# Kernel tuning notes

Measured on AMD Instinct MI355X. Metric: run time of the kernel, lower is better.

## Reference

```python
import jax, jax.numpy as jnp
import numpy as np
from jax import lax

B, C_IN, L = 16, 4, 300000
KERNEL, ANCHOR_N = 11, 16
LEAK = 1e-4
EPS = 1e-12  # torch F.normalize eps


def setup_inputs() -> dict:
    key = jax.random.key(0)
    k1, k2, k3 = jax.random.split(key, 3)
    data = jax.random.normal(k1, (B, C_IN, L), dtype=jnp.float32)
    # Conv1d weights, PyTorch default init scale ~ U(-s, s), s = 1/sqrt(fan_in)
    s = 1.0 / np.sqrt(C_IN * KERNEL)
    W = jax.random.uniform(k2, (ANCHOR_N, C_IN, KERNEL), dtype=jnp.float32, minval=-s, maxval=s)
    b = jax.random.uniform(k3, (ANCHOR_N,), dtype=jnp.float32, minval=-s, maxval=s)
    return {"data": data, "W": W, "b": b, "anchor_index": 3}


def reference(data, W, b, anchor_index):
    # Conv1d(4 -> anchor_n, valid padding) + LeakyReLU(0.0001)
    y = lax.conv_general_dilated(
        data, W, window_strides=(1,), padding="VALID",
        dimension_numbers=("NCH", "OIH", "NCH"))
    y = y + b[None, :, None]                      # [B, anchor_n, Lc]
    y = jnp.where(y > 0, y, LEAK * y)
    # select anchor channel, add leading dim -> [1, B, Lc]
    ch = y[:, anchor_index, :][None]
    # F.normalize(dim=2, p=1)
    denom = jnp.maximum(jnp.sum(jnp.abs(ch), axis=2, keepdims=True), EPS)
    channel = ch / denom
    # softmax over sequence dim (gamma = 1)
    dist = jax.nn.softmax(channel, axis=2)
    # weighted moments of position distribution (single pass each)
    Lc = dist.shape[2]
    x = jnp.arange(Lc, dtype=dist.dtype)          # positions
    mean = jnp.sum(dist * x, axis=2, keepdims=True)    # [1,B,1]
    x_diff = x - mean                                   # [1,B,Lc]
    var = jnp.sum(dist * x_diff * x_diff, axis=2, keepdims=True)
    z = x_diff / jnp.sqrt(var)
    z3 = z * z * z
    skews = jnp.mean(z3, axis=2)                  # [1,B]
    kts = jnp.mean(z3 * z, axis=2) - 3.0          # [1,B]
    return (skews, kts, channel)
```

## Files before the change

### kernel.cpp

```cpp
#include <hip/hip_runtime.h>
#include <hip/hip_cooperative_groups.h>
#include <math.h>

namespace cg = cooperative_groups;

#define BATCH 16
#define CIN 4
#define LEN 300000
#define KW 11
#define LC (LEN - KW + 1)
#define LCP 300000
#define LEAK 1e-4f
#define EPS_N 1e-12f

#define TPB 256
#define EPT 4
#define NBX 64
#define NBLK (NBX * BATCH)
#define CHUNK 4688
#define ITER 5


__device__ inline void conv_iter_fast(const float* __restrict__ src,
                                      const float* w, float sb, float* yo)
{
    float acc0 = sb, acc1 = sb, acc2 = sb, acc3 = sb;
#pragma unroll
    for (int c = 0; c < CIN; ++c) {
        const float* s = src + (size_t)c * LEN;
        const float4 v0 = *(const float4*)(s);
        const float4 v1 = *(const float4*)(s + 4);
        const float4 v2 = *(const float4*)(s + 8);
        const float4 v3 = *(const float4*)(s + 12);
        float x[16] = { v0.x, v0.y, v0.z, v0.w,  v1.x, v1.y, v1.z, v1.w,
                        v2.x, v2.y, v2.z, v2.w,  v3.x, v3.y, v3.z, v3.w };
#pragma unroll
        for (int k = 0; k < KW; ++k) {
            const float wv = w[c * KW + k];
            acc0 = fmaf(x[k],     wv, acc0);
            acc1 = fmaf(x[k + 1], wv, acc1);
            acc2 = fmaf(x[k + 2], wv, acc2);
            acc3 = fmaf(x[k + 3], wv, acc3);
        }
    }
    yo[0] = acc0 > 0.0f ? acc0 : LEAK * acc0;
    yo[1] = acc1 > 0.0f ? acc1 : LEAK * acc1;
    yo[2] = acc2 > 0.0f ? acc2 : LEAK * acc2;
    yo[3] = acc3 > 0.0f ? acc3 : LEAK * acc3;
}

__device__ inline float conv_one(const float* __restrict__ dbase, int l,
                                 const float* w, float sb)
{
    float acc = sb;
#pragma unroll
    for (int c = 0; c < CIN; ++c)
#pragma unroll
        for (int k = 0; k < KW; ++k)
            acc = fmaf(dbase[(size_t)c * LEN + l + k], w[c * KW + k], acc);
    return acc > 0.0f ? acc : LEAK * acc;
}

__device__ inline void finalize_row(double e, double m1, double m2,
                                    float* __restrict__ out, int b)
{
    const double mean = m1 / e;
    const double var  = m2 / e - mean * mean;

    const double n   = (double)LC;
    const double nm1 = n - 1.0;
    const double S1p = 0.5 * n * nm1;
    const double S2p = nm1 * n * (2.0 * n - 1.0) / 6.0;
    const double S3p = S1p * S1p;
    const double S4p = S2p * (3.0 * n * n - 3.0 * n - 1.0) / 5.0;

    const double mu  = mean;
    const double mu2 = mu * mu;
    const double P3 = S3p - 3.0 * mu * S2p + 3.0 * mu2 * S1p - n * mu * mu2;
    const double P4 = S4p - 4.0 * mu * S3p + 6.0 * mu2 * S2p
                      - 4.0 * mu * mu2 * S1p + n * mu2 * mu2;

    const double sv = sqrt(var);
    out[b]         = (float)(P3 / (n * sv * sv * sv));
    out[BATCH + b] = (float)(P4 / (n * var * var) - 3.0);
}

__global__ __launch_bounds__(256, 4) void fused(
    const float* __restrict__ data, const float* __restrict__ W,
    const float* __restrict__ bias, const int* __restrict__ aidx,
    float* __restrict__ out,
    double* __restrict__ absP, float* __restrict__ maxP, double* __restrict__ sP)
{
    cg::grid_group grid = cg::this_grid();

    const int b = blockIdx.y, j = blockIdx.x, tid = threadIdx.x;
    const int a = aidx[0];

    float w[CIN * KW];
#pragma unroll
    for (int k = 0; k < CIN * KW; ++k) w[k] = W[a * CIN * KW + k];
    const float sb = bias[a];

    const float* dbase = data + (size_t)b * (CIN * (size_t)LEN);
    const int cstart = j * CHUNK;
    const int cend   = min(cstart + CHUNK, LC);

    float y[ITER][EPT];
    float aabs = 0.0f, amax = -INFINITY;

#pragma unroll
    for (int it = 0; it < ITER; ++it) {
        const int o = cstart + it * (TPB * EPT) + tid * EPT;
        if (o + EPT <= cend && o + 16 <= LEN) {
            conv_iter_fast(dbase + o, w, sb, y[it]);
            aabs += (fabsf(y[it][0]) + fabsf(y[it][1])) +
                    (fabsf(y[it][2]) + fabsf(y[it][3]));
            amax = fmaxf(amax, fmaxf(fmaxf(y[it][0], y[it][1]),
                                     fmaxf(y[it][2], y[it][3])));
        } else {
#pragma unroll
            for (int u = 0; u < EPT; ++u) {
                const int l = o + u;
                if (l < cend) {
                    const float v = conv_one(dbase, l, w, sb);
                    y[it][u] = v;
                    aabs += fabsf(v);
                    amax = fmaxf(amax, v);
                }
            }
        }
    }

#pragma unroll
    for (int off = 32; off; off >>= 1) {
        aabs += __shfl_down(aabs, off);
        amax = fmaxf(amax, __shfl_down(amax, off));
    }
    __shared__ float ra[4], rm[4];
    const int wv = tid >> 6;
    if ((tid & 63) == 0) { ra[wv] = aabs; rm[wv] = amax; }
    __syncthreads();
    if (tid == 0) {
        absP[b * NBX + j] = (double)((ra[0] + ra[1]) + (ra[2] + ra[3]));
        maxP[b * NBX + j] = fmaxf(fmaxf(rm[0], rm[1]), fmaxf(rm[2], rm[3]));
    }

    grid.sync();

    __shared__ float sstat[2];
    if (tid < 64) {
        double s = absP[b * NBX + tid];
        float  m = maxP[b * NBX + tid];
#pragma unroll
        for (int off = 32; off; off >>= 1) {
            s += __shfl_down(s, off);
            m = fmaxf(m, __shfl_down(m, off));
        }
        if (tid == 0) {
            sstat[0] = fmaxf((float)s, EPS_N);
            sstat[1] = m;
        }
    }
    __syncthreads();
    const float inv = 1.0f / sstat[0];
    const float mx  = sstat[1] * inv;

    float* dst = out + 2 * BATCH + (size_t)b * LC;

    double te = 0.0, t1 = 0.0, t2 = 0.0;

#pragma unroll
    for (int it = 0; it < ITER; ++it) {
        const int o = cstart + it * (TPB * EPT) + tid * EPT;
        if (o + EPT <= cend && o + 16 <= LEN) {
            const float c0 = y[it][0] * inv, c1 = y[it][1] * inv;
            const float c2 = y[it][2] * inv, c3 = y[it][3] * inv;
            if ((b & 1) == 0) {
                *(float4*)(dst + o) = make_float4(c0, c1, c2, c3);
            } else {
                *(float2*)(dst + o)     = make_float2(c0, c1);
                *(float2*)(dst + o + 2) = make_float2(c2, c3);
            }
            const float e0 = expf(c0 - mx), e1 = expf(c1 - mx);
            const float e2 = expf(c2 - mx), e3 = expf(c3 - mx);
            const float se  = (e0 + e1) + (e2 + e3);
            const float su  = e1 + 2.0f * e2 + 3.0f * e3;
            const float suu = e1 + 4.0f * e2 + 9.0f * e3;
            const double od = (double)o;
            te += (double)se;
            t1 += od * (double)se + (double)su;
            t2 += od * od * (double)se + 2.0 * od * (double)su + (double)suu;
        } else {
#pragma unroll
            for (int u = 0; u < EPT; ++u) {
                const int l = o + u;
                if (l < cend) {
                    const float c = y[it][u] * inv;
                    dst[l] = c;
                    const float e = expf(c - mx);
                    const double xd = (double)l;
                    te += (double)e;
                    t1 += (double)e * xd;
                    t2 += (double)e * xd * xd;
                }
            }
        }
    }

#pragma unroll
    for (int off = 32; off; off >>= 1) {
        te += __shfl_down(te, off);
        t1 += __shfl_down(t1, off);
        t2 += __shfl_down(t2, off);
    }
    __shared__ double we[4], w1[4], w2[4];
    if ((tid & 63) == 0) { we[wv] = te; w1[wv] = t1; w2[wv] = t2; }
    __syncthreads();
    if (tid == 0) {
        double* p = sP + (size_t)(b * NBX + j) * 3;
        p[0] = (we[0] + we[1]) + (we[2] + we[3]);
        p[1] = (w1[0] + w1[1]) + (w1[2] + w1[3]);
        p[2] = (w2[0] + w2[1]) + (w2[2] + w2[3]);
    }

    grid.sync();

    if (j == 0 && tid < 64) {
        const double* p = sP + (size_t)(b * NBX + tid) * 3;
        double e = p[0], m1 = p[1], m2 = p[2];
#pragma unroll
        for (int off = 32; off; off >>= 1) {
            e  += __shfl_down(e, off);
            m1 += __shfl_down(m1, off);
            m2 += __shfl_down(m2, off);
        }
        if (tid == 0) finalize_row(e, m1, m2, out, b);
    }
}

__global__ __launch_bounds__(256) void conv_stats_fb(
    const float* __restrict__ data, const float* __restrict__ W,
    const float* __restrict__ bias, const int* __restrict__ aidx,
    float* __restrict__ ch, double* __restrict__ absP, float* __restrict__ maxP)
{
    const int b = blockIdx.y, j = blockIdx.x, tid = threadIdx.x;
    const int a = aidx[0];
    float w[CIN * KW];
#pragma unroll
    for (int k = 0; k < CIN * KW; ++k) w[k] = W[a * CIN * KW + k];
    const float sb = bias[a];

    const float* dbase = data + (size_t)b * (CIN * (size_t)LEN);
    float* chrow = ch + (size_t)b * LCP;
    const int cstart = j * CHUNK;
    const int cend   = min(cstart + CHUNK, LC);

    float aabs = 0.0f, amax = -INFINITY;
#pragma unroll
    for (int it = 0; it < ITER; ++it) {
        const int o = cstart + it * (TPB * EPT) + tid * EPT;
        if (o + EPT <= cend && o + 16 <= LEN) {
            float yv[EPT];
            conv_iter_fast(dbase + o, w, sb, yv);
            *(float4*)(chrow + o) = make_float4(yv[0], yv[1], yv[2], yv[3]);
            aabs += (fabsf(yv[0]) + fabsf(yv[1])) + (fabsf(yv[2]) + fabsf(yv[3]));
            amax = fmaxf(amax, fmaxf(fmaxf(yv[0], yv[1]), fmaxf(yv[2], yv[3])));
        } else {
            for (int l = o; l < min(o + EPT, cend); ++l) {
                const float v = conv_one(dbase, l, w, sb);
                chrow[l] = v;
                aabs += fabsf(v);
                amax = fmaxf(amax, v);
            }
        }
    }

#pragma unroll
    for (int off = 32; off; off >>= 1) {
        aabs += __shfl_down(aabs, off);
        amax = fmaxf(amax, __shfl_down(amax, off));
    }
    __shared__ float ra[4], rm[4];
    const int wv = tid >> 6;
    if ((tid & 63) == 0) { ra[wv] = aabs; rm[wv] = amax; }
    __syncthreads();
    if (tid == 0) {
        absP[b * NBX + j] = (double)((ra[0] + ra[1]) + (ra[2] + ra[3]));
        maxP[b * NBX + j] = fmaxf(fmaxf(rm[0], rm[1]), fmaxf(rm[2], rm[3]));
    }
}

__global__ __launch_bounds__(256) void softmax_fb(
    const float* __restrict__ ch, const double* __restrict__ absP,
    const float* __restrict__ maxP, float* __restrict__ chan_out,
    double* __restrict__ sP)
{
    const int b = blockIdx.y, j = blockIdx.x, tid = threadIdx.x;

    __shared__ float sstat[2];
    if (tid < 64) {
        double s = absP[b * NBX + tid];
        float  m = maxP[b * NBX + tid];
#pragma unroll
        for (int off = 32; off; off >>= 1) {
            s += __shfl_down(s, off);
            m = fmaxf(m, __shfl_down(m, off));
        }
        if (tid == 0) { sstat[0] = fmaxf((float)s, EPS_N); sstat[1] = m; }
    }
    __syncthreads();
    const float inv = 1.0f / sstat[0];
    const float mx  = sstat[1] * inv;

    const float* src = ch + (size_t)b * LCP;
    float* dst = chan_out + (size_t)b * LC;
    const int cstart = j * CHUNK;
    const int cend   = min(cstart + CHUNK, LC);

    double te = 0.0, t1 = 0.0, t2 = 0.0;
#pragma unroll
    for (int it = 0; it < ITER; ++it) {
        const int o = cstart + it * (TPB * EPT) + tid * EPT;
        if (o + EPT <= cend) {
            const float4 v = *(const float4*)(src + o);
            const float c0 = v.x * inv, c1 = v.y * inv, c2 = v.z * inv, c3 = v.w * inv;
            if ((b & 1) == 0) {
                *(float4*)(dst + o) = make_float4(c0, c1, c2, c3);
            } else {
                *(float2*)(dst + o)     = make_float2(c0, c1);
                *(float2*)(dst + o + 2) = make_float2(c2, c3);
            }
            const float e0 = expf(c0 - mx), e1 = expf(c1 - mx);
            const float e2 = expf(c2 - mx), e3 = expf(c3 - mx);
            const float se  = (e0 + e1) + (e2 + e3);
            const float su  = e1 + 2.0f * e2 + 3.0f * e3;
            const float suu = e1 + 4.0f * e2 + 9.0f * e3;
            const double od = (double)o;
            te += (double)se;
            t1 += od * (double)se + (double)su;
            t2 += od * od * (double)se + 2.0 * od * (double)su + (double)suu;
        } else {
            for (int l = o; l < cend; ++l) {
                const float c = src[l] * inv;
                dst[l] = c;
                const float e = expf(c - mx);
                const double xd = (double)l;
                te += (double)e;
                t1 += (double)e * xd;
                t2 += (double)e * xd * xd;
            }
        }
    }

#pragma unroll
    for (int off = 32; off; off >>= 1) {
        te += __shfl_down(te, off);
        t1 += __shfl_down(t1, off);
        t2 += __shfl_down(t2, off);
    }
    __shared__ double we[4], w1[4], w2[4];
    const int wv = tid >> 6;
    if ((tid & 63) == 0) { we[wv] = te; w1[wv] = t1; w2[wv] = t2; }
    __syncthreads();
    if (tid == 0) {
        double* p = sP + (size_t)(b * NBX + j) * 3;
        p[0] = (we[0] + we[1]) + (we[2] + we[3]);
        p[1] = (w1[0] + w1[1]) + (w1[2] + w1[3]);
        p[2] = (w2[0] + w2[1]) + (w2[2] + w2[3]);
    }
}

__global__ void finalize_fb(const double* __restrict__ sP, float* __restrict__ out)
{
    const int b = blockIdx.x, t = threadIdx.x;
    const double* p = sP + (size_t)(b * NBX + t) * 3;
    double te = p[0], t1 = p[1], t2 = p[2];
#pragma unroll
    for (int off = 32; off; off >>= 1) {
        te += __shfl_down(te, off);
        t1 += __shfl_down(t1, off);
        t2 += __shfl_down(t2, off);
    }
    if (t == 0) finalize_row(te, t1, t2, out, b);
}

extern "C" void kernel_launch(void* const* d_in, const int* in_sizes, int n_in,
                              void* d_out, int out_size, void* d_ws, size_t ws_size,
                              hipStream_t stream) {
    const float* data = (const float*)d_in[0];
    const float* W    = (const float*)d_in[1];
    const float* bias = (const float*)d_in[2];
    const int*   aidx = (const int*)d_in[3];
    float* out = (float*)d_out;

    char* ws = (char*)d_ws;
    double* absP = (double*)(ws + 0);
    float*  maxP = (float*) (ws + 8192);
    double* sP   = (double*)(ws + 16384);
    float*  ch   = (float*) (ws + 65536);

    int bpc = 0;
    hipError_t oe = hipOccupancyMaxActiveBlocksPerMultiprocessor(
        &bpc, (const void*)fused, TPB, 0);
    const bool coop_ok = (oe == hipSuccess) && (bpc * 256 >= NBLK);

    if (coop_ok) {
        void* args[] = { (void*)&data, (void*)&W, (void*)&bias, (void*)&aidx,
                         (void*)&out, (void*)&absP, (void*)&maxP, (void*)&sP };
        hipLaunchCooperativeKernel((const void*)fused, dim3(NBX, BATCH), dim3(TPB),
                                   args, 0, stream);
    } else {
        dim3 grid(NBX, BATCH);
        conv_stats_fb<<<grid, dim3(TPB), 0, stream>>>(data, W, bias, aidx, ch,
                                                      absP, maxP);
        softmax_fb<<<grid, dim3(TPB), 0, stream>>>(ch, absP, maxP,
                                                   out + 2 * BATCH, sP);
        finalize_fb<<<dim3(BATCH), dim3(64), 0, stream>>>(sP, out);
    }
}
```

Baseline: 133.1 us.

## Replace grid syncs with per-row atomic counters and drop softmax max pass

Replaces the two cooperative grid-wide barriers with per-batch-row atomic accumulators and arrival counters. Blocks spin only until their own row's 64 blocks finish, and the last-arriving block finalizes the row. The softmax max reduction is removed on the basis that the L1-normalized values are bounded (|c| ≤ 1), so exp needs no shift. A memset of the counter workspace is added per call, and the spin-wait relies on all blocks of a row being co-resident, which the cooperative launch still guarantees.

```diff
diff --git a/kernel.cpp b/kernel.cpp
--- a/kernel.cpp
+++ b/kernel.cpp
@@ -21,6 +21,16 @@
 #define ITER 5
 
 
+__device__ __forceinline__ double atomAddD(double* p, double v) {
+    return __hip_atomic_fetch_add(p, v, __ATOMIC_RELAXED, __HIP_MEMORY_SCOPE_AGENT);
+}
+__device__ __forceinline__ unsigned atomAddU(unsigned* p, unsigned v) {
+    return __hip_atomic_fetch_add(p, v, __ATOMIC_RELAXED, __HIP_MEMORY_SCOPE_AGENT);
+}
+__device__ __forceinline__ unsigned dep_one(long long mix) {
+    return (mix == (long long)0x8000000000000000LL) ? 2u : 1u;
+}
+
 __device__ inline void conv_iter_fast(const float* __restrict__ src,
                                       const float* w, float sb, float* yo)
 {
@@ -89,10 +99,8 @@
     const float* __restrict__ data, const float* __restrict__ W,
     const float* __restrict__ bias, const int* __restrict__ aidx,
     float* __restrict__ out,
-    double* __restrict__ absP, float* __restrict__ maxP, double* __restrict__ sP)
-{
-    cg::grid_group grid = cg::this_grid();
-
+    double* accA, unsigned* cntA, double* statB, unsigned* cntB)
+{
     const int b = blockIdx.y, j = blockIdx.x, tid = threadIdx.x;
     const int a = aidx[0];
 
@@ -106,7 +114,7 @@
     const int cend   = min(cstart + CHUNK, LC);
 
     float y[ITER][EPT];
-    float aabs = 0.0f, amax = -INFINITY;
+    float aabs = 0.0f;
 
 #pragma unroll
     for (int it = 0; it < ITER; ++it) {
@@ -115,8 +123,6 @@
             conv_iter_fast(dbase + o, w, sb, y[it]);
             aabs += (fabsf(y[it][0]) + fabsf(y[it][1])) +
                     (fabsf(y[it][2]) + fabsf(y[it][3]));
-            amax = fmaxf(amax, fmaxf(fmaxf(y[it][0], y[it][1]),
-                                     fmaxf(y[it][2], y[it][3])));
         } else {
 #pragma unroll
             for (int u = 0; u < EPT; ++u) {
@@ -125,45 +131,33 @@
                     const float v = conv_one(dbase, l, w, sb);
                     y[it][u] = v;
                     aabs += fabsf(v);
-                    amax = fmaxf(amax, v);
                 }
             }
         }
     }
 
 #pragma unroll
-    for (int off = 32; off; off >>= 1) {
-        aabs += __shfl_down(aabs, off);
-        amax = fmaxf(amax, __shfl_down(amax, off));
-    }
-    __shared__ float ra[4], rm[4];
+    for (int off = 32; off; off >>= 1) aabs += __shfl_down(aabs, off);
+    __shared__ float ra[4];
     const int wv = tid >> 6;
-    if ((tid & 63) == 0) { ra[wv] = aabs; rm[wv] = amax; }
-    __syncthreads();
+    if ((tid & 63) == 0) ra[wv] = aabs;
+    __syncthreads();
+
     if (tid == 0) {
-        absP[b * NBX + j] = (double)((ra[0] + ra[1]) + (ra[2] + ra[3]));
-        maxP[b * NBX + j] = fmaxf(fmaxf(rm[0], rm[1]), fmaxf(rm[2], rm[3]));
-    }
-
-    grid.sync();
-
-    __shared__ float sstat[2];
-    if (tid < 64) {
-        double s = absP[b * NBX + tid];
-        float  m = maxP[b * NBX + tid];
-#pragma unroll
-        for (int off = 32; off; off >>= 1) {
-            s += __shfl_down(s, off);
-            m = fmaxf(m, __shfl_down(m, off));
-        }
-        if (tid == 0) {
-            sstat[0] = fmaxf((float)s, EPS_N);
-            sstat[1] = m;
-        }
-    }
-    __syncthreads();
-    const float inv = 1.0f / sstat[0];
-    const float mx  = sstat[1] * inv;
+        const double blockSum = (double)((ra[0] + ra[1]) + (ra[2] + ra[3]));
+        const double old = atomAddD(&accA[b * 8], blockSum);
+        atomAddU(&cntA[b * 16], dep_one(__double_as_longlong(old)));
+    }
+
+    __shared__ float sden;
+    if (tid == 0) {
+        while (atomAddU(&cntA[b * 16], 0u) < (unsigned)NBX)
+            __builtin_amdgcn_s_sleep(8);
+        const double d = atomAddD(&accA[b * 8], 0.0);
+        sden = fmaxf((float)d, EPS_N);
+    }
+    __syncthreads();
+    const float inv = 1.0f / sden;
 
     float* dst = out + 2 * BATCH + (size_t)b * LC;
 
@@ -181,8 +175,8 @@
                 *(float2*)(dst + o)     = make_float2(c0, c1);
                 *(float2*)(dst + o + 2) = make_float2(c2, c3);
             }
-            const float e0 = expf(c0 - mx), e1 = expf(c1 - mx);
-            const float e2 = expf(c2 - mx), e3 = expf(c3 - mx);
+            const float e0 = expf(c0), e1 = expf(c1);
+            const float e2 = expf(c2), e3 = expf(c3);
             const float se  = (e0 + e1) + (e2 + e3);
             const float su  = e1 + 2.0f * e2 + 3.0f * e3;
             const float suu = e1 + 4.0f * e2 + 9.0f * e3;
@@ -197,7 +191,7 @@
                 if (l < cend) {
                     const float c = y[it][u] * inv;
                     dst[l] = c;
-                    const float e = expf(c - mx);
+                    const float e = expf(c);
                     const double xd = (double)l;
                     te += (double)e;
                     t1 += (double)e * xd;
@@ -216,25 +210,25 @@
     __shared__ double we[4], w1[4], w2[4];
     if ((tid & 63) == 0) { we[wv] = te; w1[wv] = t1; w2[wv] = t2; }
     __syncthreads();
+
     if (tid == 0) {
-        double* p = sP + (size_t)(b * NBX + j) * 3;
-        p[0] = (we[0] + we[1]) + (we[2] + we[3]);
-        p[1] = (w1[0] + w1[1]) + (w1[2] + w1[3]);
-        p[2] = (w2[0] + w2[1]) + (w2[2] + w2[3]);
-    }
-
-    grid.sync();
-
-    if (j == 0 && tid < 64) {
-        const double* p = sP + (size_t)(b * NBX + tid) * 3;
-        double e = p[0], m1 = p[1], m2 = p[2];
-#pragma unroll
-        for (int off = 32; off; off >>= 1) {
-            e  += __shfl_down(e, off);
-            m1 += __shfl_down(m1, off);
-            m2 += __shfl_down(m2, off);
-        }
-        if (tid == 0) finalize_row(e, m1, m2, out, b);
+        const double pe = (we[0] + we[1]) + (we[2] + we[3]);
+        const double p1 = (w1[0] + w1[1]) + (w1[2] + w1[3]);
+        const double p2 = (w2[0] + w2[1]) + (w2[2] + w2[3]);
+        double* slot = statB + (size_t)(b * 3) * 8;
+        const double o0 = atomAddD(slot + 0,  pe);
+        const double o1 = atomAddD(slot + 8,  p1);
+        const double o2 = atomAddD(slot + 16, p2);
+        const long long mix = __double_as_longlong(o0) ^
+                              __double_as_longlong(o1) ^
+                              __double_as_longlong(o2);
+        const unsigned old = atomAddU(&cntB[b * 16], dep_one(mix));
+        if (old == (unsigned)(NBX - 1)) {
+            const double e  = atomAddD(slot + 0,  0.0);
+            const double m1 = atomAddD(slot + 8,  0.0);
+            const double m2 = atomAddD(slot + 16, 0.0);
+            finalize_row(e, m1, m2, out, b);
+        }
     }
 }
 
@@ -394,10 +388,16 @@
     float* out = (float*)d_out;
 
     char* ws = (char*)d_ws;
-    double* absP = (double*)(ws + 0);
-    float*  maxP = (float*) (ws + 8192);
-    double* sP   = (double*)(ws + 16384);
-    float*  ch   = (float*) (ws + 65536);
+    double*   accA  = (double*)  (ws + 0);
+    unsigned* cntA  = (unsigned*)(ws + 1024);
+    double*   statB = (double*)  (ws + 2048);
+    unsigned* cntB  = (unsigned*)(ws + 5120);
+    double*   absP  = (double*)  (ws + 8192);
+    float*    maxP  = (float*)   (ws + 16384);
+    double*   sP    = (double*)  (ws + 24576);
+    float*    ch    = (float*)   (ws + 65536);
+
+    hipMemsetAsync(ws, 0, 6144, stream);
 
     int bpc = 0;
     hipError_t oe = hipOccupancyMaxActiveBlocksPerMultiprocessor(
@@ -406,7 +406,8 @@
 
     if (coop_ok) {
         void* args[] = { (void*)&data, (void*)&W, (void*)&bias, (void*)&aidx,
-                         (void*)&out, (void*)&absP, (void*)&maxP, (void*)&sP };
+                         (void*)&out, (void*)&accA, (void*)&cntA,
+                         (void*)&statB, (void*)&cntB };
         hipLaunchCooperativeKernel((const void*)fused, dim3(NBX, BATCH), dim3(TPB),
                                    args, 0, stream);
     } else {
```

Result: no change. 134.6 us (+1.1%).
